# Kernel tuning notes

Measured on AMD Instinct MI355X. Metric: run time of the kernel, lower is better.

## Reference

```python
import jax, jax.numpy as jnp
import numpy as np

NEG = jnp.float32(-1e30)  # finite stand-in for -inf (grad-safe)
BLANK = 0


def setup_inputs() -> dict:
    key = jax.random.key(0)
    k1, k2, k3, k4 = jax.random.split(key, 4)
    B, T, V, S = 64, 1024, 128, 256
    logits = jax.random.normal(k1, (B, T, V), dtype=jnp.float32)
    log_probs = jax.nn.log_softmax(logits, axis=-1)  # valid log-probs like a model head
    log_probs_length = jax.random.randint(k2, (B,), 768, T + 1)
    text_encoded = jax.random.randint(k3, (B, S), 1, V)  # labels exclude blank=0
    text_encoded_length = jax.random.randint(k4, (B,), 64, S + 1)
    return {
        "log_probs": log_probs,
        "log_probs_length": log_probs_length,
        "text_encoded": text_encoded,
        "text_encoded_length": text_encoded_length,
    }


def _ctc_loss(log_probs, input_lengths, targets, target_lengths):
    """CTC loss, matching torch.nn.CTCLoss(blank=0, reduction='mean', zero_infinity=True)."""
    B, T, V = log_probs.shape
    S = targets.shape[1]
    L2 = 2 * S + 1  # extended label sequence: blank-interleaved

    # extended labels ext[b, s]: blank at even s, target[(s-1)//2] at odd s
    ext = jnp.full((B, L2), BLANK, dtype=targets.dtype)
    ext = ext.at[:, 1::2].set(targets)

    # gather per-step log-prob of each extended label: [B, T, L2]
    lp_ext = jnp.take_along_axis(
        log_probs, jnp.broadcast_to(ext[:, None, :], (B, T, L2)), axis=2
    )

    pos = jnp.arange(L2)
    valid_s = pos[None, :] < (2 * target_lengths[:, None] + 1)  # [B, L2]
    ext_m2 = jnp.pad(ext, ((0, 0), (2, 0)), constant_values=BLANK)[:, :-2]
    # skip transition s-2 -> s allowed only at non-blank (odd) positions with differing labels
    skip_mask = (pos[None, :] >= 2) & (pos[None, :] % 2 == 1) & (ext != ext_m2)

    alpha0 = jnp.full((B, L2), NEG, dtype=log_probs.dtype)
    alpha0 = alpha0.at[:, 0].set(lp_ext[:, 0, 0])
    alpha0 = alpha0.at[:, 1].set(jnp.where(target_lengths > 0, lp_ext[:, 0, 1], NEG))
    alpha0 = jnp.where(valid_s, alpha0, NEG)

    lp_ext_T = jnp.moveaxis(lp_ext, 1, 0)  # [T, B, L2]

    def step(alpha, x):
        lp_t, t = x
        s1 = jnp.pad(alpha, ((0, 0), (1, 0)), constant_values=NEG)[:, :-1]
        s2 = jnp.pad(alpha, ((0, 0), (2, 0)), constant_values=NEG)[:, :-2]
        a = jnp.logaddexp(alpha, s1)
        a = jnp.where(skip_mask, jnp.logaddexp(a, s2), a)
        new = jnp.where(valid_s, a + lp_t, NEG)
        # freeze alpha for samples whose input sequence has ended
        new = jnp.where((t < input_lengths)[:, None], new, alpha)
        return new, None

    alpha, _ = jax.lax.scan(step, alpha0, (lp_ext_T[1:], jnp.arange(1, T)))

    L = target_lengths
    idx1 = (2 * L)[:, None]
    idx0 = jnp.maximum(2 * L - 1, 0)[:, None]
    a_blank = jnp.take_along_axis(alpha, idx1, axis=1)[:, 0]
    a_label = jnp.take_along_axis(alpha, idx0, axis=1)[:, 0]
    ll = jnp.logaddexp(a_blank, jnp.where(L > 0, a_label, NEG))
    loss_b = -ll
    # zero_infinity: zero out infeasible alignments
    loss_b = jnp.where(loss_b > 1e29, jnp.float32(0.0), loss_b)
    # reduction='mean': divide each loss by its target length, then batch-mean
    return jnp.mean(loss_b / jnp.maximum(L, 1).astype(log_probs.dtype))


def reference(log_probs, log_probs_length, text_encoded, text_encoded_length):
    return _ctc_loss(log_probs, log_probs_length, text_encoded, text_encoded_length)
```

## Files before the change

### kernel.cpp

```cpp
#include <hip/hip_runtime.h>

constexpr int B_ = 64;
constexpr int T_ = 1024;
constexpr int V_ = 128;
constexpr int S_ = 256;
constexpr int GRING = 32;
constexpr int ROWF = 384;
constexpr int NGW = 5;
constexpr float INV_LN2 = 1.4426950408889634f;
constexpr float LN2 = 0.6931471805599453f;

#define WG_SCOPE __HIP_MEMORY_SCOPE_WORKGROUP

__device__ __forceinline__ void poll_eq(int* p, int want) {
    while (__hip_atomic_load(p, __ATOMIC_RELAXED, WG_SCOPE) != want)
        __builtin_amdgcn_s_sleep(1);
}

__device__ __forceinline__ int wave_rescale(float a[10], int& K) {
    float mx = a[0];
    #pragma unroll
    for (int k = 1; k < 10; ++k) mx = fmaxf(mx, a[k]);
    #pragma unroll
    for (int d = 1; d < 64; d <<= 1) mx = fmaxf(mx, __shfl_xor(mx, d, 64));
    int e;
    (void)frexpf(mx, &e);
    const int ks = (mx > 0.0f) ? (124 - e) : 0;
    #pragma unroll
    for (int k = 0; k < 10; ++k) a[k] = ldexpf(a[k], ks);
    K += ks;
    return ks;
}

__global__ __launch_bounds__(768) void ctc_fused6(
    const float* __restrict__ lp,
    const int* __restrict__ in_len,
    const int* __restrict__ tgt,
    const int* __restrict__ tgt_len,
    float* __restrict__ ws)
{
    const int b    = blockIdx.x;
    const int tid  = threadIdx.x;
    const int wid  = tid >> 6;
    const int lane = tid & 63;

    __shared__ float ringF[GRING * ROWF];
    __shared__ float ringB[GRING * ROWF];
    __shared__ float dumpA[640];
    __shared__ float dumpB[640];
    __shared__ int   tagF[8], tagB[8];
    __shared__ int   consF, consB;
    __shared__ int   KFsh, KBsh;

    const int L  = tgt_len[b];
    const int Tb = in_len[b];
    const float* lpb = lp + (size_t)b * T_ * V_;
    const int* tg = tgt + b * S_;

    const int tm = (Tb - 2) >> 1;
    const int Uf = tm;
    const int Ub = Tb - 2 - tm;

    if (tid == 0) { consF = 0; consB = 0; }
    if (tid < 8) tagF[tid] = -1;
    else if (tid < 16) tagB[tid - 8] = -1;
    __syncthreads();

    if (wid >= 2) {
        const int dir = (wid - 2) / NGW;
        const int q   = (wid - 2) % NGW;
        const int U   = dir ? Ub : Uf;
        float* ring   = dir ? ringB : ringF;
        int*   tags   = dir ? tagB  : tagF;
        int*   consp  = dir ? &consB : &consF;

        int   labE[5];
        float vmask[5];
        #pragma unroll
        for (int c = 0; c < 5; ++c) {
            const int j = 5 * lane + c;
            if (j < L) { labE[c] = tg[j]; vmask[c] = 1.0f; }
            else       { labE[c] = 0;     vmask[c] = 0.0f; }
        }

        for (int m = q; 4 * m + 1 <= U; m += NGW) {
            const int n = min(4, U - 4 * m);
            float v[4][6];
            #pragma unroll
            for (int r = 0; r < 4; ++r) {
                if (r < n) {
                    const int u = 4 * m + 1 + r;
                    const int t = dir ? (Tb - 1 - u) : u;
                    const float* row = lpb + (size_t)t * V_;
                    v[r][0] = row[0];
                    #pragma unroll
                    for (int c = 0; c < 5; ++c) v[r][c + 1] = row[labE[c]];
                }
            }
            while (__hip_atomic_load(consp, __ATOMIC_RELAXED, WG_SCOPE) < 4 * m - 28)
                __builtin_amdgcn_s_sleep(1);
            #pragma unroll
            for (int r = 0; r < 4; ++r) {
                if (r < n) {
                    const int u = 4 * m + 1 + r;
                    float e[6];
                    e[0] = __builtin_exp2f(v[r][0] * INV_LN2);
                    #pragma unroll
                    for (int c = 0; c < 5; ++c)
                        e[c + 1] = vmask[c] * __builtin_exp2f(v[r][c + 1] * INV_LN2);
                    float* rb = ring + ((u - 1) & (GRING - 1)) * ROWF;
                    ((float2*)rb)[lane]         = make_float2(e[0], e[1]);
                    ((float2*)(rb + 128))[lane] = make_float2(e[2], e[3]);
                    ((float2*)(rb + 256))[lane] = make_float2(e[4], e[5]);
                }
            }
            if (lane == 0)
                __hip_atomic_store(&tags[m & 7], m, __ATOMIC_RELEASE, WG_SCOPE);
        }
    } else if (wid == 0) {
        float skipf[5];
        #pragma unroll
        for (int c = 0; c < 5; ++c) {
            const int j = 5 * lane + c;
            skipf[c] = (j >= 1 && j < L && tg[j] != tg[j - 1]) ? 1.0f : 0.0f;
        }
        float a[10];
        #pragma unroll
        for (int k = 0; k < 10; ++k) a[k] = 0.0f;
        {
            const float p00 = __builtin_exp2f(lpb[0] * INV_LN2);
            const float p01 = __builtin_exp2f(lpb[tg[0]] * INV_LN2);
            if (lane == 0) { a[0] = p00; a[1] = p01; }
        }
        float u9n = 0.0f;
        int K = 0;

        float2 S[4][12];
        auto readBlock = [&](int set, int m) {
            const int base = ((4 * m) & (GRING - 1)) * ROWF + 2 * lane;
            #pragma unroll
            for (int r = 0; r < 4; ++r)
                #pragma unroll
                for (int pl = 0; pl < 3; ++pl)
                    S[set][r * 3 + pl] =
                        *(const float2*)&ringF[base + r * ROWF + pl * 128];
        };
        auto rowCore = [&](float2 c0, float2 c1, float2 c2) {
            const float u9 = u9n;
            const float p0 = c0.x;
            a[9] = (a[9] + a[8] + skipf[4] * a[7]) * c2.y;
            const float t9 = __shfl_up(a[9], 1, 64);
            u9n = (lane == 0) ? 0.0f : t9;
            a[8] = (a[8] + a[7]) * p0;
            a[7] = (a[7] + a[6] + skipf[3] * a[5]) * c2.x;
            a[6] = (a[6] + a[5]) * p0;
            a[5] = (a[5] + a[4] + skipf[2] * a[3]) * c1.y;
            a[4] = (a[4] + a[3]) * p0;
            a[3] = (a[3] + a[2] + skipf[1] * a[1]) * c1.x;
            a[2] = (a[2] + a[1]) * p0;
            a[1] = (a[1] + a[0] + skipf[0] * u9) * c0.y;
            a[0] = (a[0] + u9) * p0;
        };
        auto row4 = [&](int set) {
            #pragma unroll
            for (int r = 0; r < 4; ++r)
                rowCore(S[set][r * 3], S[set][r * 3 + 1], S[set][r * 3 + 2]);
        };
        auto body = [&](int m, int setc, int setp) {
            if (4 * (m + 2) + 1 <= Uf) {
                poll_eq(&tagF[(m + 2) & 7], m + 2);
                readBlock(setp, m + 2);
            }
            row4(setc);
            if (lane == 0)
                __hip_atomic_store(&consF, 4 * m + 4, __ATOMIC_RELAXED, WG_SCOPE);
        };

        const int MB4 = (Uf / 4) & ~3;
        poll_eq(&tagF[0], 0); readBlock(0, 0);
        poll_eq(&tagF[1], 1); readBlock(1, 1);
        for (int mb = 0; mb < MB4; mb += 4) {
            body(mb + 0, 0, 2);
            body(mb + 1, 1, 3);
            { const int ks = wave_rescale(a, K); u9n = ldexpf(u9n, ks); }
            body(mb + 2, 2, 0);
            body(mb + 3, 3, 1);
            { const int ks = wave_rescale(a, K); u9n = ldexpf(u9n, ks); }
        }
        #pragma unroll
        for (int r = 0; r < 4; ++r)
            if (4 * MB4 + 1 + r <= Uf)
                rowCore(S[0][r * 3], S[0][r * 3 + 1], S[0][r * 3 + 2]);
        #pragma unroll
        for (int r = 0; r < 4; ++r)
            if (4 * MB4 + 5 + r <= Uf)
                rowCore(S[1][r * 3], S[1][r * 3 + 1], S[1][r * 3 + 2]);
        { const int ks = wave_rescale(a, K); u9n = ldexpf(u9n, ks); }
        for (int u = 4 * MB4 + 9; u <= Uf; ++u) {
            const int bu = (u - 1) >> 2;
            poll_eq(&tagF[bu & 7], bu);
            const int base = ((u - 1) & (GRING - 1)) * ROWF + 2 * lane;
            const float2 c0 = *(const float2*)&ringF[base];
            const float2 c1 = *(const float2*)&ringF[base + 128];
            const float2 c2 = *(const float2*)&ringF[base + 256];
            rowCore(c0, c1, c2);
        }

        #pragma unroll
        for (int k = 0; k < 10; ++k) dumpA[10 * lane + k] = a[k];
        if (lane == 0) {
            KFsh = K;
            __hip_atomic_store(&consF, Uf + 64, __ATOMIC_RELAXED, WG_SCOPE);
        }
    } else {
        float sB[5];
        #pragma unroll
        for (int c = 0; c < 5; ++c) {
            const int j = 5 * lane + c + 1;
            sB[c] = (j < L && tg[j] != tg[j - 1]) ? 1.0f : 0.0f;
        }
        float g[10];
        #pragma unroll
        for (int k = 0; k < 10; ++k) g[k] = 0.0f;
        {
            const float pb = __builtin_exp2f(lpb[(size_t)(Tb - 1) * V_] * INV_LN2);
            const float pl = __builtin_exp2f(lpb[(size_t)(Tb - 1) * V_ + tg[L - 1]] * INV_LN2);
            #pragma unroll
            for (int k = 0; k < 10; ++k) {
                const int s = 10 * lane + k;
                if (s == 2 * L)     g[k] = pb;
                if (s == 2 * L - 1) g[k] = pl;
            }
        }
        float t0 = __shfl_down(g[0], 1, 64), t1 = __shfl_down(g[1], 1, 64);
        float d0n = (lane == 63) ? 0.0f : t0;
        float d1n = (lane == 63) ? 0.0f : t1;
        int K = 0;

        float2 S[4][12];
        auto readBlock = [&](int set, int m) {
            const int base = ((4 * m) & (GRING - 1)) * ROWF + 2 * lane;
            #pragma unroll
            for (int r = 0; r < 4; ++r)
                #pragma unroll
                for (int pl = 0; pl < 3; ++pl)
                    S[set][r * 3 + pl] =
                        *(const float2*)&ringB[base + r * ROWF + pl * 128];
        };
        auto rowCore = [&](float2 c0, float2 c1, float2 c2) {
            const float d0 = d0n, d1 = d1n;
            const float p0 = c0.x;
            g[0] = (g[0] + g[1]) * p0;
            g[1] = (g[1] + g[2] + sB[0] * g[3]) * c0.y;
            const float q0 = __shfl_down(g[0], 1, 64);
            const float q1 = __shfl_down(g[1], 1, 64);
            d0n = (lane == 63) ? 0.0f : q0;
            d1n = (lane == 63) ? 0.0f : q1;
            g[2] = (g[2] + g[3]) * p0;
            g[3] = (g[3] + g[4] + sB[1] * g[5]) * c1.x;
            g[4] = (g[4] + g[5]) * p0;
            g[5] = (g[5] + g[6] + sB[2] * g[7]) * c1.y;
            g[6] = (g[6] + g[7]) * p0;
            g[7] = (g[7] + g[8] + sB[3] * g[9]) * c2.x;
            g[8] = (g[8] + g[9]) * p0;
            g[9] = (g[9] + d0 + sB[4] * d1) * c2.y;
        };
        auto row4 = [&](int set) {
            #pragma unroll
            for (int r = 0; r < 4; ++r)
                rowCore(S[set][r * 3], S[set][r * 3 + 1], S[set][r * 3 + 2]);
        };
        auto body = [&](int m, int setc, int setp) {
            if (4 * (m + 2) + 1 <= Ub) {
                poll_eq(&tagB[(m + 2) & 7], m + 2);
                readBlock(setp, m + 2);
            }
            row4(setc);
            if (lane == 0)
                __hip_atomic_store(&consB, 4 * m + 4, __ATOMIC_RELAXED, WG_SCOPE);
        };

        const int MB4 = (Ub / 4) & ~3;
        poll_eq(&tagB[0], 0); readBlock(0, 0);
        poll_eq(&tagB[1], 1); readBlock(1, 1);
        for (int mb = 0; mb < MB4; mb += 4) {
            body(mb + 0, 0, 2);
            body(mb + 1, 1, 3);
            { const int ks = wave_rescale(g, K);
              d0n = ldexpf(d0n, ks); d1n = ldexpf(d1n, ks); }
            body(mb + 2, 2, 0);
            body(mb + 3, 3, 1);
            { const int ks = wave_rescale(g, K);
              d0n = ldexpf(d0n, ks); d1n = ldexpf(d1n, ks); }
        }
        #pragma unroll
        for (int r = 0; r < 4; ++r)
            if (4 * MB4 + 1 + r <= Ub)
                rowCore(S[0][r * 3], S[0][r * 3 + 1], S[0][r * 3 + 2]);
        #pragma unroll
        for (int r = 0; r < 4; ++r)
            if (4 * MB4 + 5 + r <= Ub)
                rowCore(S[1][r * 3], S[1][r * 3 + 1], S[1][r * 3 + 2]);
        { const int ks = wave_rescale(g, K);
          d0n = ldexpf(d0n, ks); d1n = ldexpf(d1n, ks); }
        for (int u = 4 * MB4 + 9; u <= Ub; ++u) {
            const int bu = (u - 1) >> 2;
            poll_eq(&tagB[bu & 7], bu);
            const int base = ((u - 1) & (GRING - 1)) * ROWF + 2 * lane;
            const float2 c0 = *(const float2*)&ringB[base];
            const float2 c1 = *(const float2*)&ringB[base + 128];
            const float2 c2 = *(const float2*)&ringB[base + 256];
            rowCore(c0, c1, c2);
        }

        {
            const float d0 = d0n, d1 = d1n;
            g[0] = g[0] + g[1];
            g[1] = g[1] + g[2] + sB[0] * g[3];
            g[2] = g[2] + g[3];
            g[3] = g[3] + g[4] + sB[1] * g[5];
            g[4] = g[4] + g[5];
            g[5] = g[5] + g[6] + sB[2] * g[7];
            g[6] = g[6] + g[7];
            g[7] = g[7] + g[8] + sB[3] * g[9];
            g[8] = g[8] + g[9];
            g[9] = g[9] + d0 + sB[4] * d1;
        }
        #pragma unroll
        for (int k = 0; k < 10; ++k) dumpB[10 * lane + k] = g[k];
        if (lane == 0) {
            KBsh = K;
            __hip_atomic_store(&consB, Ub + 64, __ATOMIC_RELAXED, WG_SCOPE);
        }
    }

    __syncthreads();
    if (wid == 0) {
        double sum = 0.0;
        #pragma unroll
        for (int k = 0; k < 10; ++k)
            sum += (double)dumpA[10 * lane + k] * (double)dumpB[10 * lane + k];
        #pragma unroll
        for (int d = 1; d < 64; d <<= 1) sum += __shfl_xor(sum, d, 64);
        if (lane == 0) {
            float loss = 0.0f;
            if (sum > 0.0) {
                const long long ub = __double_as_longlong(sum);
                const int ex = (int)((ub >> 52) & 2047) - 1023;
                const double f = __longlong_as_double(
                    (ub & 0x000FFFFFFFFFFFFFLL) | 0x3FF0000000000000LL);
                const float ll2 = __builtin_log2f((float)f)
                                + (float)(ex - KFsh - KBsh);
                loss = -(ll2 * LN2);
                if (!(loss <= 1e29f)) loss = 0.0f;
            }
            ws[b] = loss / (float)L;
        }
    }
}

__global__ void ctc_reduce_kernel(const float* __restrict__ ws, float* __restrict__ out) {
    float v = ws[threadIdx.x];
    #pragma unroll
    for (int o = 32; o > 0; o >>= 1) v += __shfl_down(v, o);
    if (threadIdx.x == 0) out[0] = v / (float)B_;
}

extern "C" void kernel_launch(void* const* d_in, const int* in_sizes, int n_in,
                              void* d_out, int out_size, void* d_ws, size_t ws_size,
                              hipStream_t stream) {
    const float* lp      = (const float*)d_in[0];
    const int*   in_len  = (const int*)d_in[1];
    const int*   tgt     = (const int*)d_in[2];
    const int*   tgt_len = (const int*)d_in[3];
    float* loss = (float*)d_ws;
    float* out  = (float*)d_out;

    ctc_fused6<<<B_, 768, 0, stream>>>(lp, in_len, tgt, tgt_len, loss);
    ctc_reduce_kernel<<<1, 64, 0, stream>>>(loss, out);
}
```

Before: 137.7 us.

## Load coalesced log-prob rows and gather labels via wave shuffles with double-buffered prefetch

Producer waves now read each full 128-entry log-prob row as a coalesced float2 per lane and exponentiate it once. The per-label values are then gathered with cross-lane shuffles, replacing five scattered global loads per lane. Row loads are double-buffered, so the next chunk is fetched while the current one is processed. The number of producer waves per direction drops from five to three (768 to 512 threads), and the tag publish changes to a relaxed store after an explicit LDS waitcnt, which leans on hardware ordering and adds some risk.

Measured after the change: 140.3 us. Within noise of the previous version (+1.9%).

```diff
diff --git a/kernel.cpp b/kernel.cpp
--- a/kernel.cpp
+++ b/kernel.cpp
@@ -6,7 +6,7 @@
 constexpr int S_ = 256;
 constexpr int GRING = 32;
 constexpr int ROWF = 384;
-constexpr int NGW = 5;
+constexpr int NGW = 3;
 constexpr float INV_LN2 = 1.4426950408889634f;
 constexpr float LN2 = 0.6931471805599453f;
 
@@ -32,7 +32,7 @@
     return ks;
 }
 
-__global__ __launch_bounds__(768) void ctc_fused6(
+__global__ __launch_bounds__(512) void ctc_fused7(
     const float* __restrict__ lp,
     const int* __restrict__ in_len,
     const int* __restrict__ tgt,
@@ -67,55 +67,77 @@
     __syncthreads();
 
     if (wid >= 2) {
-        const int dir = (wid - 2) / NGW;
-        const int q   = (wid - 2) % NGW;
+        const int gw  = wid - 2;
+        const int dir = gw / NGW;
+        const int q   = gw % NGW;
         const int U   = dir ? Ub : Uf;
         float* ring   = dir ? ringB : ringF;
         int*   tags   = dir ? tagB  : tagF;
         int*   consp  = dir ? &consB : &consF;
 
-        int   labE[5];
+        int   perm[5], oddc[5];
         float vmask[5];
         #pragma unroll
         for (int c = 0; c < 5; ++c) {
             const int j = 5 * lane + c;
-            if (j < L) { labE[c] = tg[j]; vmask[c] = 1.0f; }
-            else       { labE[c] = 0;     vmask[c] = 0.0f; }
-        }
-
-        for (int m = q; 4 * m + 1 <= U; m += NGW) {
+            if (j < L) { const int lb = tg[j]; perm[c] = lb >> 1; oddc[c] = lb & 1; vmask[c] = 1.0f; }
+            else       { perm[c] = 0; oddc[c] = 0; vmask[c] = 0.0f; }
+        }
+
+        float2 R0[4], R1[4];
+        auto issue = [&](float2 (&Rb)[4], int m) {
             const int n = min(4, U - 4 * m);
-            float v[4][6];
             #pragma unroll
             for (int r = 0; r < 4; ++r) {
                 if (r < n) {
                     const int u = 4 * m + 1 + r;
                     const int t = dir ? (Tb - 1 - u) : u;
-                    const float* row = lpb + (size_t)t * V_;
-                    v[r][0] = row[0];
-                    #pragma unroll
-                    for (int c = 0; c < 5; ++c) v[r][c + 1] = row[labE[c]];
+                    Rb[r] = *(const float2*)(lpb + (size_t)t * V_ + 2 * lane);
                 }
             }
+        };
+        auto process = [&](float2 (&Rb)[4], int m) {
             while (__hip_atomic_load(consp, __ATOMIC_RELAXED, WG_SCOPE) < 4 * m - 28)
                 __builtin_amdgcn_s_sleep(1);
+            const int n = min(4, U - 4 * m);
             #pragma unroll
             for (int r = 0; r < 4; ++r) {
                 if (r < n) {
-                    const int u = 4 * m + 1 + r;
-                    float e[6];
-                    e[0] = __builtin_exp2f(v[r][0] * INV_LN2);
+                    const float e0 = __builtin_exp2f(Rb[r].x * INV_LN2);
+                    const float e1 = __builtin_exp2f(Rb[r].y * INV_LN2);
+                    const float b0 = __shfl(e0, 0, 64);
+                    float gv[5];
                     #pragma unroll
-                    for (int c = 0; c < 5; ++c)
-                        e[c + 1] = vmask[c] * __builtin_exp2f(v[r][c + 1] * INV_LN2);
-                    float* rb = ring + ((u - 1) & (GRING - 1)) * ROWF;
-                    ((float2*)rb)[lane]         = make_float2(e[0], e[1]);
-                    ((float2*)(rb + 128))[lane] = make_float2(e[2], e[3]);
-                    ((float2*)(rb + 256))[lane] = make_float2(e[4], e[5]);
+                    for (int c = 0; c < 5; ++c) {
+                        const float lo = __shfl(e0, perm[c], 64);
+                        const float hi = __shfl(e1, perm[c], 64);
+                        gv[c] = vmask[c] * (oddc[c] ? hi : lo);
+                    }
+                    float* rb = ring + ((4 * m + r) & (GRING - 1)) * ROWF;
+                    ((float2*)rb)[lane]         = make_float2(b0,    gv[0]);
+                    ((float2*)(rb + 128))[lane] = make_float2(gv[1], gv[2]);
+                    ((float2*)(rb + 256))[lane] = make_float2(gv[3], gv[4]);
                 }
             }
+            asm volatile("s_waitcnt lgkmcnt(0)" ::: "memory");
             if (lane == 0)
-                __hip_atomic_store(&tags[m & 7], m, __ATOMIC_RELEASE, WG_SCOPE);
+                __hip_atomic_store(&tags[m & 7], m, __ATOMIC_RELAXED, WG_SCOPE);
+        };
+
+        int m = q;
+        if (4 * m + 1 <= U) {
+            issue(R0, m);
+            if (4 * (m + NGW) + 1 <= U) issue(R1, m + NGW);
+            while (true) {
+                process(R0, m);
+                if (4 * (m + 2 * NGW) + 1 <= U) issue(R0, m + 2 * NGW);
+                m += NGW;
+                if (4 * m + 1 > U) break;
+                process(R1, m);
+                if (4 * (m + 2 * NGW) + 1 <= U) issue(R1, m + 2 * NGW);
+                m += NGW;
+                if (4 * m + 1 > U) break;
+            }
         }
     } else if (wid == 0) {
         float skipf[5];
@@ -376,6 +398,6 @@
     float* loss = (float*)d_ws;
     float* out  = (float*)d_out;
 
-    ctc_fused6<<<B_, 768, 0, stream>>>(lp, in_len, tgt, tgt_len, loss);
+    ctc_fused7<<<B_, 512, 0, stream>>>(lp, in_len, tgt, tgt_len, loss);
     ctc_reduce_kernel<<<1, 64, 0, stream>>>(loss, out);
 }
```
